# Performance work log

Hardware: AMD Instinct MI355X
Metric: run time of the kernel (lower is better)

The kernel has to match this reference:

```python
import jax, jax.numpy as jnp
import numpy as np

DIM = 1024
HEADS = 16
DIM_HEAD = 64
B = 16
N = 512
INNER = HEADS * DIM_HEAD            # 1024
CPB_DIM = DIM // 2                  # 512
INNER_FF = int(DIM * 4 * 2 / 3)     # 2730
EPS = 1e-5


def setup_inputs() -> dict:
    key = jax.random.key(0)
    ks = jax.random.split(key, 10)
    s = lambda i, shape, scale: jax.random.normal(ks[i], shape, jnp.float32) * scale
    return dict(
        x=s(0, (B, N, DIM), 1.0),
        g_ln=jnp.ones((DIM,), jnp.float32),
        Wq=s(1, (DIM, INNER), 0.02),
        Wkv=s(2, (DIM, 2 * INNER), 0.02),
        Wo=s(3, (INNER, DIM), 0.02),
        cpb_w1=s(4, (1, CPB_DIM), 0.5),
        cpb_b1=jnp.zeros((CPB_DIM,), jnp.float32),
        cpb_w2=s(5, (CPB_DIM, CPB_DIM), 0.05),
        cpb_b2=jnp.zeros((CPB_DIM,), jnp.float32),
        cpb_w3=s(6, (CPB_DIM, HEADS), 0.05),
        cpb_b3=jnp.zeros((HEADS,), jnp.float32),
        ff_w_in=s(7, (2 * INNER_FF, DIM), 0.02),
        ff_g=jnp.ones((INNER_FF,), jnp.float32),
        ff_w_out=s(8, (DIM, INNER_FF), 0.02),
    )


def _seq_ln(x, g):
    # Faithful to repo's LayerNorm: mean/var over dim=1 (sequence axis of [b,n,d])
    mean = jnp.mean(x, axis=1, keepdims=True)
    var = jnp.var(x, axis=1, keepdims=True)  # unbiased=False
    return (x - mean) * jax.lax.rsqrt(jnp.maximum(var, EPS)) * g


def reference(x, g_ln, Wq, Wkv, Wo, cpb_w1, cpb_b1, cpb_w2, cpb_b2, cpb_w3, cpb_b3,
              ff_w_in, ff_g, ff_w_out):
    b, n, d = x.shape
    # ContinuousPositionBias (1D, 2 layers)
    pos = jnp.arange(n, dtype=jnp.float32)
    rel = (pos[:, None] - pos[None, :])[..., None]           # [n,n,1]
    rel = jnp.sign(rel) * jnp.log(jnp.abs(rel) + 1.0)        # log-distance
    h = jax.nn.silu(rel @ cpb_w1 + cpb_b1)
    h = jax.nn.silu(h @ cpb_w2 + cpb_b2)
    bias = (h @ cpb_w3 + cpb_b3).transpose(2, 0, 1)          # [h,n,n]

    # Attention (framerate=None -> no pos_embeds; context = x)
    xn = _seq_ln(x, g_ln)
    q = xn @ Wq
    k, v = jnp.split(xn @ Wkv, 2, axis=-1)
    to_heads = lambda t: t.reshape(b, n, HEADS, DIM_HEAD).transpose(0, 2, 1, 3)
    q, k, v = to_heads(q), to_heads(k), to_heads(v)
    q = q * (DIM_HEAD ** -0.5)
    sim = jnp.einsum('bhid,bhjd->bhij', q, k) + bias[None]
    attn = jax.nn.softmax(sim, axis=-1)
    o = jnp.einsum('bhij,bhjd->bhid', attn, v)
    o = o.transpose(0, 2, 1, 3).reshape(b, n, INNER)
    x = jnp.nan_to_num(o @ Wo) + x

    # FeedForward: Conv1d(k=1) -> GEGLU -> ChanLayerNorm -> Conv1d(k=1), residual
    xt = x.transpose(0, 2, 1)                                # [b,d,n]
    hff = jnp.einsum('oc,bcn->bon', ff_w_in, xt)             # [b,2*inner_ff,n]
    x1, gate = jnp.split(hff, 2, axis=1)
    hff = x1 * jax.nn.gelu(gate, approximate=False)
    mean = jnp.mean(hff, axis=1, keepdims=True)
    var = jnp.var(hff, axis=1, keepdims=True)
    hff = (hff - mean) * jax.lax.rsqrt(jnp.maximum(var, EPS)) * ff_g[None, :, None]
    out = jnp.einsum('oc,bcn->bon', ff_w_out, hff).transpose(0, 2, 1) + x
    return out
```

## Files before the change

kernel.cpp:

```cpp
#include <hip/hip_runtime.h>

#define DEV __device__ __forceinline__

typedef __attribute__((ext_vector_type(8))) short bf16x8;
typedef __attribute__((ext_vector_type(4))) float f32x4;

DEV float b2f(unsigned short u) { union { unsigned int i; float f; } v; v.i = ((unsigned)u) << 16; return v.f; }
DEV unsigned short f2b(float f) {
    union { float f; unsigned int i; } v; v.f = f;
    unsigned r = v.i + 0x7FFFu + ((v.i >> 16) & 1u);
    return (unsigned short)(r >> 16);
}

DEV void llds16(const unsigned short* g, unsigned short* l) {
    __builtin_amdgcn_global_load_lds((const __attribute__((address_space(1))) void*)g,
                                     (__attribute__((address_space(3))) void*)l, 16, 0, 0);
}

__global__ __launch_bounds__(256) void transpose_cast_k(const float* __restrict__ src,
        unsigned short* __restrict__ dst, int Nc, int K, float scale)
{
    __shared__ float tile[32][33];
    int tx = threadIdx.x, ty = threadIdx.y;
    int c0 = blockIdx.x * 32;
    int r0 = blockIdx.y * 32;
#pragma unroll
    for (int r = 0; r < 4; r++)
        tile[ty + r * 8][tx] = src[(size_t)(r0 + ty + r * 8) * Nc + c0 + tx];
    __syncthreads();
#pragma unroll
    for (int r = 0; r < 4; r++)
        dst[(size_t)(c0 + ty + r * 8) * K + r0 + tx] = f2b(tile[tx][ty + r * 8] * scale);
}

__global__ __launch_bounds__(256) void cast_wfin_k(const float* __restrict__ src,
        unsigned short* __restrict__ dst)
{
    int idx = blockIdx.x * 256 + threadIdx.x;
    int nr = idx >> 8;
    int c4 = (idx & 255) * 4;
    int chunk = nr >> 5, which = (nr >> 4) & 1, pos = nr & 15;
    int c = chunk * 16 + pos;
    unsigned short o0 = 0, o1 = 0, o2 = 0, o3 = 0;
    if (c < 2730) {
        const float* s = src + (size_t)(which * 2730 + c) * 1024 + c4;
        o0 = f2b(s[0]); o1 = f2b(s[1]); o2 = f2b(s[2]); o3 = f2b(s[3]);
    }
    unsigned short* d = dst + (size_t)nr * 1024 + c4;
    d[0] = o0; d[1] = o1; d[2] = o2; d[3] = o3;
}

__global__ __launch_bounds__(256) void cast_wfout_k(const float* __restrict__ src,
        unsigned short* __restrict__ dst)
{
    int idx = blockIdx.x * 256 + threadIdx.x;
    int r = idx / 2752, c = idx % 2752;
    float v = (c < 2730) ? src[(size_t)r * 2730 + c] : 0.f;
    dst[idx] = f2b(v);
}

__global__ __launch_bounds__(512) void cpb_k(const float* __restrict__ w1, const float* __restrict__ b1,
        const float* __restrict__ w2, const float* __restrict__ b2,
        const float* __restrict__ w3, const float* __restrict__ b3,
        float* __restrict__ btbl)
{
    __shared__ float sH[512];
    __shared__ float sH2[512];
    int t = threadIdx.x, row = blockIdx.x;
    int dd = row - 511;
    float ad = fabsf((float)dd);
    float sgn = (dd > 0) ? 1.f : ((dd < 0) ? -1.f : 0.f);
    float rel = sgn * logf(ad + 1.f);
    float h1 = rel * w1[t] + b1[t];
    h1 = h1 / (1.f + __expf(-h1));
    sH[t] = h1;
    __syncthreads();
    float a = b2[t];
    for (int k = 0; k < 512; k++) a += sH[k] * w2[(size_t)k * 512 + t];
    a = a / (1.f + __expf(-a));
    sH2[t] = a;
    __syncthreads();
    if (t < 16) {
        float s = b3[t];
        for (int k = 0; k < 512; k++) s += sH2[k] * w3[k * 16 + t];
        btbl[t * 1023 + row] = s;
    }
}

__global__ __launch_bounds__(256) void ln_stat_k(const float* __restrict__ x,
        float* __restrict__ part_s, float* __restrict__ part_q)
{
    int b = blockIdx.x >> 4, nc = blockIdx.x & 15, t = threadIdx.x;
    const float* xp = x + ((size_t)b * 512 + nc * 32) * 1024;
#pragma unroll
    for (int dc = 0; dc < 4; dc++) {
        int d = dc * 256 + t;
        float s = 0.f, q = 0.f;
#pragma unroll 8
        for (int n = 0; n < 32; n++) { float v = xp[(size_t)n * 1024 + d]; s += v; q += v * v; }
        part_s[((size_t)b * 16 + nc) * 1024 + d] = s;
        part_q[((size_t)b * 16 + nc) * 1024 + d] = q;
    }
}

__global__ __launch_bounds__(256) void ln_reduce_k(const float* __restrict__ part_s,
        const float* __restrict__ part_q, const float* __restrict__ gln,
        float* __restrict__ mean, float* __restrict__ inv)
{
    int b = blockIdx.x >> 2, d = (blockIdx.x & 3) * 256 + threadIdx.x;
    float s = 0.f, q = 0.f;
#pragma unroll
    for (int c = 0; c < 16; c++) {
        s += part_s[((size_t)b * 16 + c) * 1024 + d];
        q += part_q[((size_t)b * 16 + c) * 1024 + d];
    }
    float m = s * (1.f / 512.f);
    float var = q * (1.f / 512.f) - m * m;
    mean[b * 1024 + d] = m;
    inv[b * 1024 + d] = rsqrtf(fmaxf(var, 1e-5f)) * gln[d];
}

__global__ __launch_bounds__(256) void ln_apply_k(const float* __restrict__ x,
        const float* __restrict__ mean, const float* __restrict__ inv,
        unsigned short* __restrict__ xn)
{
    int b = blockIdx.x >> 4, nc = blockIdx.x & 15, t = threadIdx.x;
    const float* xp = x + ((size_t)b * 512 + nc * 32) * 1024;
    unsigned short* op = xn + ((size_t)b * 512 + nc * 32) * 1024;
#pragma unroll
    for (int dc = 0; dc < 4; dc++) {
        int d = dc * 256 + t;
        float m = mean[b * 1024 + d], iv = inv[b * 1024 + d];
#pragma unroll 8
        for (int n = 0; n < 32; n++)
            op[(size_t)n * 1024 + d] = f2b((xp[(size_t)n * 1024 + d] - m) * iv);
    }
}

__global__ __launch_bounds__(256) void gemm_bt128_k(const unsigned short* __restrict__ A,
        const unsigned short* __restrict__ BT, unsigned short* __restrict__ C,
        float* __restrict__ OUTF, const float* __restrict__ RESF,
        const unsigned short* __restrict__ RESB, int K, int ldc, int mode)
{
    __shared__ __align__(16) unsigned short lds[8192];
    int t = threadIdx.x, lane = t & 63, w = t >> 6;
    int m0 = blockIdx.x * 128, n0 = blockIdx.y * 128;
    int wm = (w >> 1) * 64, wn = (w & 1) * 64;
    int lm = lane & 15, lq = lane >> 4;
    int srow = t >> 2, scol = (t & 3) * 8;
    const unsigned short* gA0 = A + (size_t)(m0 + srow) * K + scol;
    const unsigned short* gB0 = BT + (size_t)(n0 + srow) * K + scol;
    const size_t rstep = (size_t)64 * K;
    unsigned short* l0 = &lds[w * 512];

    f32x4 acc[4][4];
#pragma unroll
    for (int i = 0; i < 4; i++)
#pragma unroll
        for (int j = 0; j < 4; j++) acc[i][j] = (f32x4){0.f, 0.f, 0.f, 0.f};

    for (int kk = 0; kk < K; kk += 32) {
        __syncthreads();
        llds16(gA0 + kk, l0);
        llds16(gA0 + rstep + kk, l0 + 2048);
        llds16(gB0 + kk, l0 + 4096);
        llds16(gB0 + rstep + kk, l0 + 6144);
        __syncthreads();
        bf16x8 af[4], bfr[4];
#pragma unroll
        for (int i = 0; i < 4; i++) af[i] = *(const bf16x8*)&lds[(wm + i * 16 + lm) * 32 + lq * 8];
#pragma unroll
        for (int j = 0; j < 4; j++) bfr[j] = *(const bf16x8*)&lds[4096 + (wn + j * 16 + lm) * 32 + lq * 8];
#pragma unroll
        for (int i = 0; i < 4; i++)
#pragma unroll
            for (int j = 0; j < 4; j++)
                acc[i][j] = __builtin_amdgcn_mfma_f32_16x16x32_bf16(af[i], bfr[j], acc[i][j], 0, 0, 0);
    }

#pragma unroll
    for (int i = 0; i < 4; i++)
#pragma unroll
        for (int j = 0; j < 4; j++)
#pragma unroll
            for (int r = 0; r < 4; r++) {
                int row = m0 + wm + i * 16 + lq * 4 + r;
                int col = n0 + wn + j * 16 + lm;
                size_t idx = (size_t)row * ldc + col;
                float v = acc[i][j][r];
                if (mode == 1) v += RESF[idx];
                if (mode == 2) { v += b2f(RESB[idx]); OUTF[idx] = v; }
                else C[idx] = f2b(v);
            }
}

__global__ __launch_bounds__(256, 2) void gemm_ffin_k(const unsigned short* __restrict__ A,
        const unsigned short* __restrict__ BT, unsigned short* __restrict__ HFFG, int K)
{
    __shared__ __align__(16) unsigned short sA[8192];
    __shared__ __align__(16) unsigned short sB[4096];
    int t = threadIdx.x, lane = t & 63, w = t >> 6;
    int m0 = blockIdx.x * 256, n0 = blockIdx.y * 128;
    int wm = (w >> 1) * 128, wn = (w & 1) * 64;
    int lm = lane & 15, lq = lane >> 4;
    int lrow4 = lane >> 2, lch = lane & 3;
    const unsigned short* gA = A + (size_t)(m0 + w * 64 + lrow4) * K + lch * 8;
    const unsigned short* gB = BT + (size_t)(n0 + w * 32 + lrow4) * K + lch * 8;

    f32x4 acc[8][4];
#pragma unroll
    for (int i = 0; i < 8; i++)
#pragma unroll
        for (int j = 0; j < 4; j++) acc[i][j] = (f32x4){0.f, 0.f, 0.f, 0.f};

    for (int kk = 0; kk < K; kk += 32) {
        __syncthreads();
#pragma unroll
        for (int c = 0; c < 4; c++)
            llds16(gA + (size_t)c * 16 * K + kk, &sA[(w * 4 + c) * 512]);
#pragma unroll
        for (int c = 0; c < 2; c++)
            llds16(gB + (size_t)c * 16 * K + kk, &sB[(w * 2 + c) * 512]);
        __syncthreads();
        bf16x8 af[8], bf[4];
#pragma unroll
        for (int i = 0; i < 8; i++) af[i] = *(const bf16x8*)&sA[(wm + i * 16 + lm) * 32 + lq * 8];
#pragma unroll
        for (int j = 0; j < 4; j++) bf[j] = *(const bf16x8*)&sB[(wn + j * 16 + lm) * 32 + lq * 8];
#pragma unroll
        for (int i = 0; i < 8; i++)
#pragma unroll
            for (int j = 0; j < 4; j++)
                acc[i][j] = __builtin_amdgcn_mfma_f32_16x16x32_bf16(af[i], bf[j], acc[i][j], 0, 0, 0);
    }

#pragma unroll
    for (int i = 0; i < 8; i++)
#pragma unroll
        for (int p = 0; p < 2; p++) {
            int c = (blockIdx.y * 4 + (wn >> 5) + p) * 16 + lm;
#pragma unroll
            for (int r = 0; r < 4; r++) {
                int row = m0 + wm + i * 16 + lq * 4 + r;
                float x1 = acc[i][2 * p][r];
                float gt = acc[i][2 * p + 1][r];
                float ge = 0.5f * gt * (1.f + erff(gt * 0.70710678118f));
                HFFG[(size_t)row * 2752 + c] = f2b(x1 * ge);
            }
        }
}

__global__ __launch_bounds__(256) void vtrans_k(const unsigned short* __restrict__ qkv,
        unsigned short* __restrict__ vT)
{
    __shared__ unsigned short sT[64 * 72];
    int t = threadIdx.x;
    int jt = blockIdx.x, bh = blockIdx.y;
    int b = bh >> 4, h = bh & 15;
#pragma unroll
    for (int it = 0; it < 16; it++) {
        int idx = it * 256 + t;
        int jl = idx >> 6, d = idx & 63;
        sT[d * 72 + jl] = qkv[((size_t)(b * 512 + jt * 64 + jl)) * 3072 + 2048 + h * 64 + d];
    }
    __syncthreads();
#pragma unroll
    for (int it = 0; it < 16; it++) {
        int idx = it * 256 + t;
        int d = idx >> 6, jl = idx & 63;
        vT[((size_t)(bh * 64 + d)) * 512 + jt * 64 + jl] = sT[d * 72 + jl];
    }
}

__global__ __launch_bounds__(256) void attn_k(const unsigned short* __restrict__ qkv,
        const unsigned short* __restrict__ vT, const float* __restrict__ btbl,
        unsigned short* __restrict__ attno)
{
    __shared__ __align__(16) unsigned short sQ[8192];
    __shared__ __align__(16) unsigned short sK[8192];
    __shared__ __align__(16) unsigned short sVT[8192];
    __shared__ __align__(16) unsigned short sP[8192];
    __shared__ float sB[1024];
    int t = threadIdx.x, lane = t & 63, w = t >> 6;
    int qt = blockIdx.x, h = blockIdx.y, b = blockIdx.z;
    int lm = lane & 15, lq = lane >> 4;
    int bh = b * 16 + h;
    int lrow4 = lane >> 2, lch = lane & 3;

    for (int i = t; i < 1023; i += 256) sB[i] = btbl[h * 1023 + i];

#pragma unroll
    for (int c = 0; c < 4; c++) {
        int cidx = w * 4 + c;
        int panel = cidx >> 3, r0 = (cidx & 7) * 16;
        const unsigned short* g = qkv + ((size_t)(b * 512 + qt * 128 + r0 + lrow4)) * 3072
                                  + h * 64 + panel * 32 + lch * 8;
        llds16(g, &sQ[panel * 4096 + r0 * 32]);
    }

    f32x4 o[2][4];
    float mrow[2][4], lrow[2][4];
#pragma unroll
    for (int it = 0; it < 2; it++)
#pragma unroll
        for (int z = 0; z < 4; z++) o[it][z] = (f32x4){0.f, 0.f, 0.f, 0.f};
#pragma unroll
    for (int it = 0; it < 2; it++)
#pragma unroll
        for (int r = 0; r < 4; r++) { mrow[it][r] = -3.0e38f; lrow[it][r] = 0.f; }

    __syncthreads();

    bf16x8 aq[2][2];
#pragma unroll
    for (int it = 0; it < 2; it++)
#pragma unroll
        for (int kh = 0; kh < 2; kh++)
            aq[it][kh] = *(const bf16x8*)&sQ[kh * 4096 + (w * 32 + it * 16 + lm) * 32 + lq * 8];

    for (int jj = 0; jj < 4; jj++) {
        __syncthreads();
#pragma unroll
        for (int c = 0; c < 4; c++) {
            int cidx = w * 4 + c;
            int panel = cidx >> 3, r0 = (cidx & 7) * 16;
            const unsigned short* g = qkv + ((size_t)(b * 512 + jj * 128 + r0 + lrow4)) * 3072
                                      + 1024 + h * 64 + panel * 32 + lch * 8;
            llds16(g, &sK[panel * 4096 + r0 * 32]);
        }
#pragma unroll
        for (int c = 0; c < 4; c++) {
            int cidx = w * 4 + c;
            int panel = cidx >> 2, d0 = (cidx & 3) * 16;
            const unsigned short* g = vT + ((size_t)(bh * 64 + d0 + lrow4)) * 512
                                      + jj * 128 + panel * 32 + lch * 8;
            llds16(g, &sVT[panel * 2048 + d0 * 32]);
        }
        __syncthreads();

#pragma unroll
        for (int ch2 = 0; ch2 < 2; ch2++) {
            f32x4 s[2][4];
#pragma unroll
            for (int it = 0; it < 2; it++)
#pragma unroll
                for (int jt = 0; jt < 4; jt++) {
                    int jl = ch2 * 64 + jt * 16 + lm;
                    f32x4 c0 = {0.f, 0.f, 0.f, 0.f};
                    c0 = __builtin_amdgcn_mfma_f32_16x16x32_bf16(aq[it][0],
                            *(const bf16x8*)&sK[jl * 32 + lq * 8], c0, 0, 0, 0);
                    c0 = __builtin_amdgcn_mfma_f32_16x16x32_bf16(aq[it][1],
                            *(const bf16x8*)&sK[4096 + jl * 32 + lq * 8], c0, 0, 0, 0);
                    s[it][jt] = c0;
                }
            int jbase = jj * 128 + ch2 * 64;
#pragma unroll
            for (int it = 0; it < 2; it++) {
                int ibase = qt * 128 + w * 32 + it * 16;
#pragma unroll
                for (int r = 0; r < 4; r++) {
                    int ip = ibase + lq * 4 + r + 511 - jbase - lm;
                    float v0 = s[it][0][r] + sB[ip];
                    float v1 = s[it][1][r] + sB[ip - 16];
                    float v2 = s[it][2][r] + sB[ip - 32];
                    float v3 = s[it][3][r] + sB[ip - 48];
                    float mx = fmaxf(fmaxf(v0, v1), fmaxf(v2, v3));
#pragma unroll
                    for (int off = 8; off > 0; off >>= 1) mx = fmaxf(mx, __shfl_xor(mx, off));
                    float mnew = fmaxf(mrow[it][r], mx);
                    float p0 = __expf(v0 - mnew);
                    float p1 = __expf(v1 - mnew);
                    float p2 = __expf(v2 - mnew);
                    float p3 = __expf(v3 - mnew);
                    float ssum = (p0 + p1) + (p2 + p3);
#pragma unroll
                    for (int off = 8; off > 0; off >>= 1) ssum += __shfl_xor(ssum, off);
                    float alpha = __expf(mrow[it][r] - mnew);
                    mrow[it][r] = mnew;
                    lrow[it][r] = lrow[it][r] * alpha + ssum;
#pragma unroll
                    for (int dt = 0; dt < 4; dt++) o[it][dt][r] *= alpha;
                    int rowl = it * 16 + lq * 4 + r;
                    unsigned short* pp = &sP[w * 2048 + rowl * 64 + lm];
                    pp[0]  = f2b(p0);
                    pp[16] = f2b(p1);
                    pp[32] = f2b(p2);
                    pp[48] = f2b(p3);
                }
            }
#pragma unroll
            for (int it = 0; it < 2; it++)
#pragma unroll
                for (int kh = 0; kh < 2; kh++) {
                    bf16x8 ap = *(const bf16x8*)&sP[w * 2048 + (it * 16 + lm) * 64 + kh * 32 + lq * 8];
#pragma unroll
                    for (int dt = 0; dt < 4; dt++) {
                        bf16x8 bv = *(const bf16x8*)&sVT[(ch2 * 2 + kh) * 2048 + (dt * 16 + lm) * 32 + lq * 8];
                        o[it][dt] = __builtin_amdgcn_mfma_f32_16x16x32_bf16(ap, bv, o[it][dt], 0, 0, 0);
                    }
                }
        }
    }

#pragma unroll
    for (int it = 0; it < 2; it++)
#pragma unroll
        for (int r = 0; r < 4; r++) {
            float inv = 1.f / lrow[it][r];
            int row = b * 512 + qt * 128 + w * 32 + it * 16 + lq * 4 + r;
#pragma unroll
            for (int dt = 0; dt < 4; dt++)
                attno[(size_t)row * 1024 + h * 64 + dt * 16 + lm] = f2b(o[it][dt][r] * inv);
        }
}

__global__ __launch_bounds__(256) void chanln_k(const unsigned short* __restrict__ hffg,
        const float* __restrict__ ffg, unsigned short* __restrict__ hffn)
{
    int row = blockIdx.x, t = threadIdx.x;
    const unsigned short* rp = hffg + (size_t)row * 2752;
    float g[11]; float sum = 0.f, ss = 0.f;
#pragma unroll
    for (int k = 0; k < 11; k++) {
        int c = t + k * 256; float v = 0.f;
        if (c < 2730) { v = b2f(rp[c]); sum += v; ss += v * v; }
        g[k] = v;
    }
#pragma unroll
    for (int off = 32; off > 0; off >>= 1) { sum += __shfl_xor(sum, off); ss += __shfl_xor(ss, off); }
    __shared__ float rb[8];
    int w = t >> 6;
    if ((t & 63) == 0) { rb[w] = sum; rb[4 + w] = ss; }
    __syncthreads();
    sum = rb[0] + rb[1] + rb[2] + rb[3];
    ss = rb[4] + rb[5] + rb[6] + rb[7];
    float mean = sum * (1.f / 2730.f);
    float var = ss * (1.f / 2730.f) - mean * mean;
    float inv = rsqrtf(fmaxf(var, 1e-5f));
    unsigned short* op = hffn + (size_t)row * 2752;
#pragma unroll
    for (int k = 0; k < 11; k++) {
        int c = t + k * 256;
        if (c < 2730) op[c] = f2b((g[k] - mean) * inv * ffg[c]);
        else if (c < 2752) op[c] = 0;
    }
}

extern "C" void kernel_launch(void* const* d_in, const int* in_sizes, int n_in,
                              void* d_out, int out_size, void* d_ws, size_t ws_size,
                              hipStream_t stream) {
    const float* x      = (const float*)d_in[0];
    const float* g_ln   = (const float*)d_in[1];
    const float* Wq     = (const float*)d_in[2];
    const float* Wkv    = (const float*)d_in[3];
    const float* Wo     = (const float*)d_in[4];
    const float* cw1    = (const float*)d_in[5];
    const float* cb1    = (const float*)d_in[6];
    const float* cw2    = (const float*)d_in[7];
    const float* cb2    = (const float*)d_in[8];
    const float* cw3    = (const float*)d_in[9];
    const float* cb3    = (const float*)d_in[10];
    const float* ffwin  = (const float*)d_in[11];
    const float* ffg    = (const float*)d_in[12];
    const float* ffwout = (const float*)d_in[13];

    char* ws = (char*)d_ws;
    unsigned short* xn    = (unsigned short*)(ws + 0);
    unsigned short* wqkvT = (unsigned short*)(ws + 16777216);
    unsigned short* woT   = (unsigned short*)(ws + 23068672);
    unsigned short* qkv   = (unsigned short*)(ws + 25165824);
    unsigned short* vT    = (unsigned short*)(ws + 75497472);
    unsigned short* attno = (unsigned short*)(ws + 92274688);
    unsigned short* hffg  = (unsigned short*)(ws + 0);
    unsigned short* wfin  = (unsigned short*)(ws + 109051904);
    unsigned short* wfout = (unsigned short*)(ws + 120324096);
    float*          btbl  = (float*)(ws + 125960192);
    unsigned short* x2b   = (unsigned short*)(ws + 126025728);
    unsigned short* hffn  = (unsigned short*)(ws + 142802944);
    float*          part_s = (float*)(ws + 187891712);
    float*          part_q = (float*)(ws + 188940288);
    float*          lnmean = (float*)(ws + 189988864);
    float*          lninv  = (float*)(ws + 190054400);

    dim3 tb(32, 8);
    transpose_cast_k<<<dim3(32, 32), tb, 0, stream>>>(Wq, wqkvT, 1024, 1024, 0.125f);
    transpose_cast_k<<<dim3(64, 32), tb, 0, stream>>>(Wkv, wqkvT + (size_t)1024 * 1024, 2048, 1024, 1.0f);
    transpose_cast_k<<<dim3(32, 32), tb, 0, stream>>>(Wo, woT, 1024, 1024, 1.0f);
    cast_wfin_k<<<5504, 256, 0, stream>>>(ffwin, wfin);
    cast_wfout_k<<<11008, 256, 0, stream>>>(ffwout, wfout);
    cpb_k<<<1023, 512, 0, stream>>>(cw1, cb1, cw2, cb2, cw3, cb3, btbl);
    ln_stat_k<<<256, 256, 0, stream>>>(x, part_s, part_q);
    ln_reduce_k<<<64, 256, 0, stream>>>(part_s, part_q, g_ln, lnmean, lninv);
    ln_apply_k<<<256, 256, 0, stream>>>(x, lnmean, lninv, xn);
    gemm_bt128_k<<<dim3(64, 24), 256, 0, stream>>>(xn, wqkvT, qkv, nullptr, nullptr, nullptr, 1024, 3072, 0);
    vtrans_k<<<dim3(8, 256), 256, 0, stream>>>(qkv, vT);
    attn_k<<<dim3(4, 16, 16), 256, 0, stream>>>(qkv, vT, btbl, attno);
    gemm_bt128_k<<<dim3(64, 8), 256, 0, stream>>>(attno, woT, x2b, nullptr, x, nullptr, 1024, 1024, 1);
    gemm_ffin_k<<<dim3(32, 43), 256, 0, stream>>>(x2b, wfin, hffg, 1024);
    chanln_k<<<8192, 256, 0, stream>>>(hffg, ffg, hffn);
    gemm_bt128_k<<<dim3(64, 8), 256, 0, stream>>>(hffn, wfout, nullptr, (float*)d_out, nullptr, x2b, 2752, 1024, 2);
}
```

Measured before the change: 648.4 us.

## Fold channel LayerNorm into FF-out GEMM epilogue and use tanh GELU

The channel LayerNorm is rewritten algebraically. Its gain is folded into the FF-out weights, a per-output-channel weight sum is precomputed, and the mean/inv-std correction moves into the final GEMM epilogue. The chanln kernel becomes a stats-only kernel, which removes writing and re-reading the normalized 8192x2752 bf16 activation. The exact erf GELU is also replaced with a tanh approximation using __expf, which cuts epilogue cost but changes numerics. The folded form computes inv*(sum x*w*g) - mu*inv*sum(w*g), which can lose precision to cancellation when the mean is large.

```diff
diff --git a/kernel.cpp b/kernel.cpp
--- a/kernel.cpp
+++ b/kernel.cpp
@@ -15,6 +15,12 @@
 DEV void llds16(const unsigned short* g, unsigned short* l) {
     __builtin_amdgcn_global_load_lds((const __attribute__((address_space(1))) void*)g,
                                      (__attribute__((address_space(3))) void*)l, 16, 0, 0);
+}
+
+DEV float gelu_f(float x) {
+    float y = 0.7978845608f * (x + 0.044715f * x * x * x);
+    float th = 1.f - 2.f / (__expf(2.f * y) + 1.f);
+    return 0.5f * x * (1.f + th);
 }
 
 __global__ __launch_bounds__(256) void transpose_cast_k(const float* __restrict__ src,
@@ -50,13 +56,24 @@
     d[0] = o0; d[1] = o1; d[2] = o2; d[3] = o3;
 }
 
-__global__ __launch_bounds__(256) void cast_wfout_k(const float* __restrict__ src,
-        unsigned short* __restrict__ dst)
+__global__ __launch_bounds__(256) void cast_wfoutg_k(const float* __restrict__ src,
+        const float* __restrict__ g, unsigned short* __restrict__ dst)
 {
     int idx = blockIdx.x * 256 + threadIdx.x;
     int r = idx / 2752, c = idx % 2752;
-    float v = (c < 2730) ? src[(size_t)r * 2730 + c] : 0.f;
+    float v = (c < 2730) ? src[(size_t)r * 2730 + c] * g[c] : 0.f;
     dst[idx] = f2b(v);
+}
+
+__global__ __launch_bounds__(64) void wgsum_k(const float* __restrict__ w,
+        const float* __restrict__ g, float* __restrict__ wgs)
+{
+    int o = blockIdx.x, t = threadIdx.x;
+    float s = 0.f;
+    for (int c = t; c < 2730; c += 64) s += w[(size_t)o * 2730 + c] * g[c];
+#pragma unroll
+    for (int off = 32; off > 0; off >>= 1) s += __shfl_xor(s, off);
+    if (t == 0) wgs[o] = s;
 }
 
 __global__ __launch_bounds__(512) void cpb_k(const float* __restrict__ w1, const float* __restrict__ b1,
@@ -140,7 +157,9 @@
 __global__ __launch_bounds__(256) void gemm_bt128_k(const unsigned short* __restrict__ A,
         const unsigned short* __restrict__ BT, unsigned short* __restrict__ C,
         float* __restrict__ OUTF, const float* __restrict__ RESF,
-        const unsigned short* __restrict__ RESB, int K, int ldc, int mode)
+        const unsigned short* __restrict__ RESB,
+        const float* __restrict__ MU, const float* __restrict__ INVV,
+        const float* __restrict__ WGS, int K, int ldc, int mode)
 {
     __shared__ __align__(16) unsigned short lds[8192];
     int t = threadIdx.x, lane = t & 63, w = t >> 6;
@@ -189,8 +208,11 @@
                 size_t idx = (size_t)row * ldc + col;
                 float v = acc[i][j][r];
                 if (mode == 1) v += RESF[idx];
-                if (mode == 2) { v += b2f(RESB[idx]); OUTF[idx] = v; }
-                else C[idx] = f2b(v);
+                if (mode == 2) {
+                    float iv = INVV[row];
+                    v = v * iv - MU[row] * iv * WGS[col] + b2f(RESB[idx]);
+                    OUTF[idx] = v;
+                } else C[idx] = f2b(v);
             }
 }
 
@@ -244,8 +266,7 @@
                 int row = m0 + wm + i * 16 + lq * 4 + r;
                 float x1 = acc[i][2 * p][r];
                 float gt = acc[i][2 * p + 1][r];
-                float ge = 0.5f * gt * (1.f + erff(gt * 0.70710678118f));
-                HFFG[(size_t)row * 2752 + c] = f2b(x1 * ge);
+                HFFG[(size_t)row * 2752 + c] = f2b(x1 * gelu_f(gt));
             }
         }
 }
@@ -414,17 +435,16 @@
         }
 }
 
-__global__ __launch_bounds__(256) void chanln_k(const unsigned short* __restrict__ hffg,
-        const float* __restrict__ ffg, unsigned short* __restrict__ hffn)
+__global__ __launch_bounds__(256) void chstat_k(const unsigned short* __restrict__ hffg,
+        float* __restrict__ mu, float* __restrict__ inv)
 {
     int row = blockIdx.x, t = threadIdx.x;
     const unsigned short* rp = hffg + (size_t)row * 2752;
-    float g[11]; float sum = 0.f, ss = 0.f;
+    float sum = 0.f, ss = 0.f;
 #pragma unroll
     for (int k = 0; k < 11; k++) {
-        int c = t + k * 256; float v = 0.f;
-        if (c < 2730) { v = b2f(rp[c]); sum += v; ss += v * v; }
-        g[k] = v;
+        int c = t + k * 256;
+        if (c < 2730) { float v = b2f(rp[c]); sum += v; ss += v * v; }
     }
 #pragma unroll
     for (int off = 32; off > 0; off >>= 1) { sum += __shfl_xor(sum, off); ss += __shfl_xor(ss, off); }
@@ -432,17 +452,13 @@
     int w = t >> 6;
     if ((t & 63) == 0) { rb[w] = sum; rb[4 + w] = ss; }
     __syncthreads();
-    sum = rb[0] + rb[1] + rb[2] + rb[3];
-    ss = rb[4] + rb[5] + rb[6] + rb[7];
-    float mean = sum * (1.f / 2730.f);
-    float var = ss * (1.f / 2730.f) - mean * mean;
-    float inv = rsqrtf(fmaxf(var, 1e-5f));
-    unsigned short* op = hffn + (size_t)row * 2752;
-#pragma unroll
-    for (int k = 0; k < 11; k++) {
-        int c = t + k * 256;
-        if (c < 2730) op[c] = f2b((g[k] - mean) * inv * ffg[c]);
-        else if (c < 2752) op[c] = 0;
+    if (t == 0) {
+        sum = rb[0] + rb[1] + rb[2] + rb[3];
+        ss = rb[4] + rb[5] + rb[6] + rb[7];
+        float m = sum * (1.f / 2730.f);
+        float var = ss * (1.f / 2730.f) - m * m;
+        mu[row] = m;
+        inv[row] = rsqrtf(fmaxf(var, 1e-5f));
     }
 }
 
@@ -476,27 +492,33 @@
     unsigned short* wfout = (unsigned short*)(ws + 120324096);
     float*          btbl  = (float*)(ws + 125960192);
     unsigned short* x2b   = (unsigned short*)(ws + 126025728);
-    unsigned short* hffn  = (unsigned short*)(ws + 142802944);
-    float*          part_s = (float*)(ws + 187891712);
-    float*          part_q = (float*)(ws + 188940288);
-    float*          lnmean = (float*)(ws + 189988864);
-    float*          lninv  = (float*)(ws + 190054400);
+    float*          part_s = (float*)(ws + 142802944);
+    float*          part_q = (float*)(ws + 143851520);
+    float*          lnmean = (float*)(ws + 144900096);
+    float*          lninv  = (float*)(ws + 144965632);
+    float*          chmu   = (float*)(ws + 145031168);
+    float*          chinv  = (float*)(ws + 145063936);
+    float*          wgs    = (float*)(ws + 145096704);
 
     dim3 tb(32, 8);
     transpose_cast_k<<<dim3(32, 32), tb, 0, stream>>>(Wq, wqkvT, 1024, 1024, 0.125f);
     transpose_cast_k<<<dim3(64, 32), tb, 0, stream>>>(Wkv, wqkvT + (size_t)1024 * 1024, 2048, 1024, 1.0f);
     transpose_cast_k<<<dim3(32, 32), tb, 0, stream>>>(Wo, woT, 1024, 1024, 1.0f);
     cast_wfin_k<<<5504, 256, 0, stream>>>(ffwin, wfin);
-    cast_wfout_k<<<11008, 256, 0, stream>>>(ffwout, wfout);
+    cast_wfoutg_k<<<11008, 256, 0, stream>>>(ffwout, ffg, wfout);
+    wgsum_k<<<1024, 64, 0, stream>>>(ffwout, ffg, wgs);
     cpb_k<<<1023, 512, 0, stream>>>(cw1, cb1, cw2, cb2, cw3, cb3, btbl);
     ln_stat_k<<<256, 256, 0, stream>>>(x, part_s, part_q);
     ln_reduce_k<<<64, 256, 0, stream>>>(part_s, part_q, g_ln, lnmean, lninv);
     ln_apply_k<<<256, 256, 0, stream>>>(x, lnmean, lninv, xn);
-    gemm_bt128_k<<<dim3(64, 24), 256, 0, stream>>>(xn, wqkvT, qkv, nullptr, nullptr, nullptr, 1024, 3072, 0);
+    gemm_bt128_k<<<dim3(64, 24), 256, 0, stream>>>(xn, wqkvT, qkv, nullptr, nullptr, nullptr,
+                                                   nullptr, nullptr, nullptr, 1024, 3072, 0);
     vtrans_k<<<dim3(8, 256), 256, 0, stream>>>(qkv, vT);
     attn_k<<<dim3(4, 16, 16), 256, 0, stream>>>(qkv, vT, btbl, attno);
-    gemm_bt128_k<<<dim3(64, 8), 256, 0, stream>>>(attno, woT, x2b, nullptr, x, nullptr, 1024, 1024, 1);
+    gemm_bt128_k<<<dim3(64, 8), 256, 0, stream>>>(attno, woT, x2b, nullptr, x, nullptr,
+                                                  nullptr, nullptr, nullptr, 1024, 1024, 1);
     gemm_ffin_k<<<dim3(32, 43), 256, 0, stream>>>(x2b, wfin, hffg, 1024);
-    chanln_k<<<8192, 256, 0, stream>>>(hffg, ffg, hffn);
-    gemm_bt128_k<<<dim3(64, 8), 256, 0, stream>>>(hffn, wfout, nullptr, (float*)d_out, nullptr, x2b, 2752, 1024, 2);
-}
+    chstat_k<<<8192, 256, 0, stream>>>(hffg, chmu, chinv);
+    gemm_bt128_k<<<dim3(64, 8), 256, 0, stream>>>(hffg, wfout, nullptr, (float*)d_out, nullptr, x2b,
+                                                  chmu, chinv, wgs, 2752, 1024, 2);
+}
```

New measurement: 651.7 us. No clear change (+0.5%).
